# Optimization experiments

Measured on AMD Instinct MI355X. Metric: run time of the kernel, lower is better.

## Reference

```python
import jax, jax.numpy as jnp
import numpy as np

D_MODEL = 512
NUM_HEADS = 8
HEAD_DIM = D_MODEL // NUM_HEADS
SEQ_LEN = 4096
BATCH = 2
D_FF = 4 * D_MODEL
EPS = 1e-5


def _layer_norm(x, g, b):
    mu = jnp.mean(x, axis=-1, keepdims=True)
    var = jnp.var(x, axis=-1, keepdims=True)
    return (x - mu) * jax.lax.rsqrt(var + EPS) * g + b


def setup_inputs() -> dict:
    key = jax.random.key(0)
    ks = jax.random.split(key, 12)
    s = 0.02
    inp = {
        "x": jax.random.normal(ks[0], (BATCH, SEQ_LEN, D_MODEL), jnp.float32),
        # Linear weights stored as [in, out] (y = x @ W + b)
        "Wq": jax.random.normal(ks[1], (D_MODEL, D_MODEL), jnp.float32) * s,
        "bq": jnp.zeros((D_MODEL,), jnp.float32),
        "Wk": jax.random.normal(ks[2], (D_MODEL, D_MODEL), jnp.float32) * s,
        "bk": jnp.zeros((D_MODEL,), jnp.float32),
        "Wv": jax.random.normal(ks[3], (D_MODEL, D_MODEL), jnp.float32) * s,
        "bv": jnp.zeros((D_MODEL,), jnp.float32),
        "Wo": jax.random.normal(ks[4], (D_MODEL, D_MODEL), jnp.float32) * s,
        "bo": jnp.zeros((D_MODEL,), jnp.float32),
        "ln1_g": jnp.ones((D_MODEL,), jnp.float32),
        "ln1_b": jnp.zeros((D_MODEL,), jnp.float32),
        "ln2_g": jnp.ones((D_MODEL,), jnp.float32),
        "ln2_b": jnp.zeros((D_MODEL,), jnp.float32),
        "W1": jax.random.normal(ks[5], (D_MODEL, D_FF), jnp.float32) * s,
        "b1": jnp.zeros((D_FF,), jnp.float32),
        "W2": jax.random.normal(ks[6], (D_FF, D_MODEL), jnp.float32) * s,
        "b2": jnp.zeros((D_MODEL,), jnp.float32),
    }
    return inp


def reference(x, Wq, bq, Wk, bk, Wv, bv, Wo, bo, ln1_g, ln1_b, ln2_g, ln2_b, W1, b1, W2, b2):
    B, S, D = x.shape
    residual = x
    h = _layer_norm(x, ln1_g, ln1_b)
    # project and split heads: [B, H, S, Dh]
    def split_heads(t):
        return t.reshape(B, S, NUM_HEADS, HEAD_DIM).transpose(0, 2, 1, 3)
    q = split_heads(h @ Wq + bq)
    k = split_heads(h @ Wk + bk)
    v = split_heads(h @ Wv + bv)
    scores = jnp.einsum("bhqd,bhkd->bhqk", q, k) / (HEAD_DIM ** 0.5)
    attn = jax.nn.softmax(scores, axis=-1)
    out = jnp.einsum("bhqk,bhkd->bhqd", attn, v)
    out = out.transpose(0, 2, 1, 3).reshape(B, S, D)
    out = out @ Wo + bo
    x1 = residual + out
    h2 = _layer_norm(x1, ln2_g, ln2_b)
    ff = jax.nn.gelu(h2 @ W1 + b1, approximate=False) @ W2 + b2
    return x1 + ff
```

## Files before the change

kernel.cpp:

```cpp
#include <hip/hip_runtime.h>
#include <hip/hip_bf16.h>
#include <math.h>

typedef __hip_bfloat16 bf16;

#define D_MODEL 512
#define NUM_HEADS 8
#define HEAD_DIM 64
#define SEQ_LEN 4096
#define BATCH 2
#define D_FF 2048
#define TOKENS (BATCH * SEQ_LEN)
#define QKV_STRIDE 1536
#define KSPLIT 2

typedef short short4v __attribute__((ext_vector_type(4)));
typedef short short8v __attribute__((ext_vector_type(8)));
typedef float float4v __attribute__((ext_vector_type(4)));
typedef float float2v __attribute__((ext_vector_type(2)));

union frag_u { short8v v8; short4v v4[2]; short s[8]; };
union pack_u { unsigned u[2]; short4v v4; };

__device__ __forceinline__ float b2f(bf16 v) { return __bfloat162float(v); }
__device__ __forceinline__ bf16 f2b(float v) { return __float2bfloat16(v); }
__device__ __forceinline__ short f2bs(float v) { bf16 t = __float2bfloat16(v); return *(short*)&t; }
__device__ __forceinline__ float exp2fast(float x) { return __builtin_amdgcn_exp2f(x); }

__device__ __forceinline__ unsigned pack_bf16(float lo, float hi) {
    unsigned a = __float_as_uint(hi) + 0x8000u;
    unsigned b = __float_as_uint(lo) + 0x8000u;
    return __builtin_amdgcn_perm(a, b, 0x07060302u);
}

__device__ __forceinline__ unsigned cvt_pk_bf16(float lo, float hi) {
    unsigned r;
    asm("v_cvt_pk_bf16_f32 %0, %1, %2" : "=v"(r) : "v"(lo), "v"(hi));
    return r;
}

__device__ __forceinline__ int3 swz_xyz() {
    int gx = gridDim.x, gy = gridDim.y;
    int id = blockIdx.x + gx * (blockIdx.y + gy * blockIdx.z);
    int nwg = gx * gy * (int)gridDim.z;
    int nid = (id & 7) * (nwg >> 3) + (id >> 3);
    int3 r;
    r.x = nid % gx;
    int t = nid / gx;
    r.y = t % gy;
    r.z = t / gy;
    return r;
}

#define AS1(p) ((__attribute__((address_space(1))) void*)(p))
#define AS3(p) ((__attribute__((address_space(3))) void*)(p))

__device__ __forceinline__ int self_detect(const unsigned* __restrict__ xw, int tid) {
    unsigned w = xw[tid & 63];
    unsigned e = (w >> 7) & 0xFFu;
    unsigned long long b = __ballot(e >= 110 && e <= 140);
    return __popcll(b) < 32;
}

__device__ __forceinline__ void do_tr(const void* __restrict__ src, bf16* __restrict__ dst,
                                      int K, int N, int n0, int k0, int fl, int tid,
                                      bf16 (*tile)[65]) {
    int c = tid & 63, r4 = tid >> 6;
#pragma unroll
    for (int t = 0; t < 16; t++) {
        int r = t * 4 + r4;
        size_t si = (size_t)(k0 + r) * N + n0 + c;
        float v = fl ? ((const float*)src)[si] : b2f(((const bf16*)src)[si]);
        tile[r][c] = f2b(v);
    }
    __syncthreads();
#pragma unroll
    for (int t = 0; t < 16; t++) {
        int r = t * 4 + r4;
        dst[(size_t)(n0 + r) * K + k0 + c] = tile[c][r];
    }
}

__global__ void prep_kernel(const void* x, const void* Wq, const void* Wk, const void* Wv,
                            const void* Wo, const void* W1, const void* W2,
                            const void* bq, const void* bk, const void* bv, const void* bo,
                            const void* b1, const void* b2,
                            const void* g1, const void* e1, const void* g2, const void* e2,
                            bf16* __restrict__ Wqkvt ,
                            bf16* __restrict__ W1t, bf16* __restrict__ W2t,
                            bf16* __restrict__ small, int* __restrict__ flag) {
    __shared__ bf16 tile[64][65];
    int blk = blockIdx.x, tid = threadIdx.x;
    int fl = self_detect((const unsigned*)x, tid);
    if (blk == 0 && tid == 0) flag[0] = fl;
    if (blk < 256) {
        int z = blk >> 6, tt = blk & 63;
        const void* src = (z == 0) ? Wq : (z == 1) ? Wk : (z == 2) ? Wv : Wo;
        do_tr(src, Wqkvt + (size_t)z * 512 * 512, 512, 512, (tt & 7) * 64, (tt >> 3) * 64,
              fl, tid, tile);
    } else if (blk < 512) {
        int tt = blk - 256;
        do_tr(W1, W1t, 512, 2048, (tt & 31) * 64, (tt >> 5) * 64, fl, tid, tile);
    } else if (blk < 768) {
        int tt = blk - 512;
        do_tr(W2, W2t, 2048, 512, (tt & 7) * 64, (tt >> 3) * 64, fl, tid, tile);
    } else {
        int i = (blk - 768) * 256 + tid;
        const void* src; int off;
        if (i < 512)       { src = bq; off = 0; }
        else if (i < 1024) { src = bk; off = 512; }
        else if (i < 1536) { src = bv; off = 1024; }
        else if (i < 2048) { src = bo; off = 1536; }
        else if (i < 4096) { src = b1; off = 2048; }
        else if (i < 4608) { src = b2; off = 4096; }
        else if (i < 5120) { src = g1; off = 4608; }
        else if (i < 5632) { src = e1; off = 5120; }
        else if (i < 6144) { src = g2; off = 5632; }
        else               { src = e2; off = 6144; }
        int j = i - off;
        small[i] = fl ? f2b(((const float*)src)[j]) : ((const bf16*)src)[j];
    }
}

template <int MODE>
__global__ void ln_kernel(const void* __restrict__ xv, const bf16* __restrict__ g,
                          const bf16* __restrict__ b, bf16* __restrict__ out,
                          const int* __restrict__ flag) {
    int t = blockIdx.x;
    int tid = threadIdx.x;
    int fl = (MODE == 2) ? *flag : 0;
    float v0, v1;
    if (fl) {
        const float* xr = (const float*)xv + (size_t)t * D_MODEL;
        v0 = xr[tid]; v1 = xr[tid + 256];
    } else {
        const bf16* xr = (const bf16*)xv + (size_t)t * D_MODEL;
        v0 = b2f(xr[tid]); v1 = b2f(xr[tid + 256]);
    }
    float s = v0 + v1, ss = v0 * v0 + v1 * v1;
    for (int o = 32; o > 0; o >>= 1) {
        s += __shfl_down(s, o);
        ss += __shfl_down(ss, o);
    }
    __shared__ float rs[4], rss[4], stat[2];
    int w = tid >> 6, l = tid & 63;
    if (l == 0) { rs[w] = s; rss[w] = ss; }
    __syncthreads();
    if (tid == 0) {
        float S = rs[0] + rs[1] + rs[2] + rs[3];
        float SS = rss[0] + rss[1] + rss[2] + rss[3];
        float mu = S / (float)D_MODEL;
        float var = SS / (float)D_MODEL - mu * mu;
        stat[0] = mu;
        stat[1] = rsqrtf(var + 1e-5f);
    }
    __syncthreads();
    float mu = stat[0], rstd = stat[1];
    bf16* orow = out + (size_t)t * D_MODEL;
    orow[tid]       = f2b((v0 - mu) * rstd * b2f(g[tid])       + b2f(b[tid]));
    orow[tid + 256] = f2b((v1 - mu) * rstd * b2f(g[tid + 256]) + b2f(b[tid + 256]));
}

__device__ __forceinline__ float gelu_tanh(float v) {
    float u = 0.7978845608f * (v + 0.044715f * v * v * v);
    float e2 = __expf(-2.f * u);
    return v / (1.f + e2);
}

template <int ACT>
__global__ __launch_bounds__(256) void mfma_gemm(
    const bf16* __restrict__ A, const bf16* __restrict__ Wt,
    const bf16* __restrict__ bias, bf16* __restrict__ Cout,
    bf16* __restrict__ Vt_out, int M, int N, int K) {
    __shared__ bf16 As[128 * 64];
    __shared__ bf16 Bs[128 * 64];
    int tid = threadIdx.x, wave = tid >> 6, lane = tid & 63;
    int m = lane & 15, g = lane >> 4;
    int3 sw = swz_xyz();
    int row0 = sw.y * 128, col0 = sw.x * 128;
    int R0 = (wave >> 1) * 64, C0 = (wave & 1) * 64;
    float4v acc[4][4] = {};

    int srow = lane >> 3;
    int scol = (lane & 7) * 8;
    const bf16* Ab = A  + (size_t)(row0 + wave * 8 + srow) * K + scol;
    const bf16* Bb = Wt + (size_t)(col0 + wave * 8 + srow) * K + scol;

    for (int k0 = 0; k0 < K; k0 += 64) {
#pragma unroll
        for (int t = 0; t < 4; t++) {
            int rbase = t * 32 + wave * 8;
            __builtin_amdgcn_global_load_lds(AS1(Ab + (size_t)(t * 32) * K + k0),
                                             AS3(&As[rbase * 64]), 16, 0, 0);
            __builtin_amdgcn_global_load_lds(AS1(Bb + (size_t)(t * 32) * K + k0),
                                             AS3(&Bs[rbase * 64]), 16, 0, 0);
        }
        __syncthreads();
#pragma unroll
        for (int kk = 0; kk < 2; kk++) {
            short8v fa[4], fb[4];
#pragma unroll
            for (int i = 0; i < 4; i++)
                fa[i] = *(const short8v*)&As[(R0 + i * 16 + m) * 64 + kk * 32 + g * 8];
#pragma unroll
            for (int j = 0; j < 4; j++)
                fb[j] = *(const short8v*)&Bs[(C0 + j * 16 + m) * 64 + kk * 32 + g * 8];
#pragma unroll
            for (int i = 0; i < 4; i++)
#pragma unroll
                for (int j = 0; j < 4; j++)
                    acc[i][j] = __builtin_amdgcn_mfma_f32_16x16x32_bf16(fa[i], fb[j], acc[i][j], 0, 0, 0);
        }
        __syncthreads();
    }

    if (Vt_out != nullptr && col0 >= 1024) {
#pragma unroll
        for (int i = 0; i < 4; i++) {
            int row = row0 + R0 + i * 16 + g * 4;
            int b = row >> 12, s = row & (SEQ_LEN - 1);
#pragma unroll
            for (int j = 0; j < 4; j++) {
                int col = col0 + C0 + j * 16 + m;
                int hh = (col - 1024) >> 6, d = col & 63;
                float bi = b2f(bias[col]);
                pack_u oo;
                oo.u[0] = pack_bf16(acc[i][j][0] + bi, acc[i][j][1] + bi);
                oo.u[1] = pack_bf16(acc[i][j][2] + bi, acc[i][j][3] + bi);
                *(short4v*)&Vt_out[((size_t)((b << 3) + hh) * 64 + d) * SEQ_LEN + s] = oo.v4;
            }
        }
        return;
    }

#pragma unroll
    for (int i = 0; i < 4; i++) {
#pragma unroll
        for (int r = 0; r < 4; r++) {
            int row = row0 + R0 + i * 16 + g * 4 + r;
#pragma unroll
            for (int j = 0; j < 4; j++) {
                int col = col0 + C0 + j * 16 + m;
                float v = acc[i][j][r] + b2f(bias[col]);
                if (ACT == 1) v = gelu_tanh(v);
                Cout[(size_t)row * N + col] = f2b(v);
            }
        }
    }
}

template <int RES, int OUTMODE>
__global__ __launch_bounds__(256) void mfma_gemm64(
    const bf16* __restrict__ A, const bf16* __restrict__ Wt,
    const bf16* __restrict__ bias, const void* __restrict__ res,
    void* __restrict__ Cout, const int* __restrict__ flag, int M, int N, int K) {
    __shared__ bf16 As[128 * 64];
    __shared__ bf16 Bs[64 * 64];
    int tid = threadIdx.x, wave = tid >> 6, lane = tid & 63;
    int m = lane & 15, g = lane >> 4;
    int3 sw = swz_xyz();
    int row0 = sw.y * 128, col0 = sw.x * 64;
    int R0 = wave * 32;
    int fl = (OUTMODE == 2 || RES == 3) ? *flag : 0;
    float4v acc[2][4] = {};

    int srow = lane >> 3;
    int scol = (lane & 7) * 8;
    const bf16* Ab = A  + (size_t)(row0 + wave * 8 + srow) * K + scol;
    const bf16* Bb = Wt + (size_t)(col0 + wave * 8 + srow) * K + scol;

    for (int k0 = 0; k0 < K; k0 += 64) {
#pragma unroll
        for (int t = 0; t < 4; t++) {
            __builtin_amdgcn_global_load_lds(AS1(Ab + (size_t)(t * 32) * K + k0),
                                             AS3(&As[(t * 32 + wave * 8) * 64]), 16, 0, 0);
            if (t < 2)
                __builtin_amdgcn_global_load_lds(AS1(Bb + (size_t)(t * 32) * K + k0),
                                                 AS3(&Bs[(t * 32 + wave * 8) * 64]), 16, 0, 0);
        }
        __syncthreads();
#pragma unroll
        for (int kk = 0; kk < 2; kk++) {
            short8v fa[2], fb[4];
#pragma unroll
            for (int i = 0; i < 2; i++)
                fa[i] = *(const short8v*)&As[(R0 + i * 16 + m) * 64 + kk * 32 + g * 8];
#pragma unroll
            for (int j = 0; j < 4; j++)
                fb[j] = *(const short8v*)&Bs[(j * 16 + m) * 64 + kk * 32 + g * 8];
#pragma unroll
            for (int i = 0; i < 2; i++)
#pragma unroll
                for (int j = 0; j < 4; j++)
                    acc[i][j] = __builtin_amdgcn_mfma_f32_16x16x32_bf16(fa[i], fb[j], acc[i][j], 0, 0, 0);
        }
        __syncthreads();
    }

#pragma unroll
    for (int i = 0; i < 2; i++) {
#pragma unroll
        for (int r = 0; r < 4; r++) {
            int row = row0 + R0 + i * 16 + g * 4 + r;
#pragma unroll
            for (int j = 0; j < 4; j++) {
                int col = col0 + j * 16 + m;
                float v = acc[i][j][r] + b2f(bias[col]);
                size_t idx = (size_t)row * N + col;
                if (RES == 2) v += b2f(((const bf16*)res)[idx]);
                if (RES == 3) v += fl ? ((const float*)res)[idx]
                                      : b2f(((const bf16*)res)[idx]);
                if (OUTMODE == 0) ((bf16*)Cout)[idx] = f2b(v);
                else {
                    if (fl) ((float*)Cout)[idx] = v;
                    else ((bf16*)Cout)[idx] = f2b(v);
                }
            }
        }
    }
}

#define F3(a, b, c) fmaxf(fmaxf((a), (b)), (c))
__global__ __launch_bounds__(256, 4) void flash_attn(const bf16* __restrict__ Q,
                                                     const bf16* __restrict__ K,
                                                     const bf16* __restrict__ Vt_g,
                                                     bf16* __restrict__ Op,
                                                     float2* __restrict__ mlout) {
    __shared__ bf16 Ks[64][72];
    __shared__ bf16 Vt[64][72];
    __shared__ bf16 Pt[4][32][72];

    int tid = threadIdx.x;
    int wave = tid >> 6, lane = tid & 63;
    int m = lane & 15, g = lane >> 4;

    int3 sw = swz_xyz();
    int bh = sw.y;
    size_t base = (size_t)(bh >> 3) * SEQ_LEN * QKV_STRIDE + (size_t)(bh & 7) * HEAD_DIM;
    int q0w = sw.x * 128 + wave * 32;

    const float qscale = 0.125f * 1.44269504f;
    short8v aQ[2][2];
#pragma unroll
    for (int mt = 0; mt < 2; mt++) {
        const bf16* qp = Q + base + (size_t)(q0w + mt * 16 + m) * QKV_STRIDE + g * 8;
#pragma unroll
        for (int c = 0; c < 2; c++) {
            frag_u u;
#pragma unroll
            for (int j = 0; j < 8; j++) u.s[j] = f2bs(b2f(qp[c * 32 + j]) * qscale);
            aQ[mt][c] = u.v8;
        }
    }

    float mrow[2] = {-1e30f, -1e30f};
    float lrow[2] = {0.f, 0.f};
    float4v oacc[2][4] = {};

    int sk = tid >> 2, sd = (tid & 3) * 16;
    int vrow = tid >> 2, vcol = (tid & 3) * 16;

    const unsigned short* Ku = (const unsigned short*)(K + base);
    const unsigned short* Vg = (const unsigned short*)Vt_g +
                               (size_t)bh * 64 * SEQ_LEN + (size_t)vrow * SEQ_LEN;

    int t0 = sw.z * (64 / KSPLIT);
    int t1 = t0 + 64 / KSPLIT;

    short8v rk0, rk1, rv0, rv1;
    {
        int kt0 = t0 * 64;
        const unsigned short* kp = Ku + (size_t)(kt0 + sk) * QKV_STRIDE + sd;
        rk0 = *(const short8v*)(kp);
        rk1 = *(const short8v*)(kp + 8);
        rv0 = *(const short8v*)(Vg + kt0 + vcol);
        rv1 = *(const short8v*)(Vg + kt0 + vcol + 8);
        *(short8v*)&Ks[sk][sd]     = rk0;
        *(short8v*)&Ks[sk][sd + 8] = rk1;
        *(short8v*)&Vt[vrow][vcol]     = rv0;
        *(short8v*)&Vt[vrow][vcol + 8] = rv1;
    }
    __syncthreads();

    for (int t = t0; t < t1; t++) {
        if (t + 1 < t1) {
            int ktn = (t + 1) * 64;
            const unsigned short* kp = Ku + (size_t)(ktn + sk) * QKV_STRIDE + sd;
            rk0 = *(const short8v*)(kp);
            rk1 = *(const short8v*)(kp + 8);
            rv0 = *(const short8v*)(Vg + ktn + vcol);
            rv1 = *(const short8v*)(Vg + ktn + vcol + 8);
        }

        float4v st[2][4];
        __builtin_amdgcn_s_setprio(1);
#pragma unroll
        for (int kt = 0; kt < 4; kt++) {
            short8v bK0 = *(const short8v*)&Ks[kt * 16 + m][g * 8];
            short8v bK1 = *(const short8v*)&Ks[kt * 16 + m][32 + g * 8];
#pragma unroll
            for (int mt = 0; mt < 2; mt++) {
                float4v a = {0.f, 0.f, 0.f, 0.f};
                a = __builtin_amdgcn_mfma_f32_16x16x32_bf16(bK0, aQ[mt][0], a, 0, 0, 0);
                a = __builtin_amdgcn_mfma_f32_16x16x32_bf16(bK1, aQ[mt][1], a, 0, 0, 0);
                st[mt][kt] = a;
            }
        }
        __builtin_amdgcn_s_setprio(0);

#pragma unroll
        for (int mt = 0; mt < 2; mt++) {
            float u0 = F3(st[mt][0][0], st[mt][0][1], st[mt][0][2]);
            float u1 = F3(st[mt][0][3], st[mt][1][0], st[mt][1][1]);
            float u2 = F3(st[mt][1][2], st[mt][1][3], st[mt][2][0]);
            float u3 = F3(st[mt][2][1], st[mt][2][2], st[mt][2][3]);
            float u4 = F3(st[mt][3][0], st[mt][3][1], st[mt][3][2]);
            float tm = fmaxf(F3(u0, u1, u2), F3(u3, u4, st[mt][3][3]));
            tm = fmaxf(tm, __shfl_xor(tm, 16));
            tm = fmaxf(tm, __shfl_xor(tm, 32));
            if (!__all(tm - mrow[mt] <= 8.f)) {
                float mnew = fmaxf(mrow[mt], tm);
                float alpha = exp2fast(mrow[mt] - mnew);
                mrow[mt] = mnew;
                lrow[mt] *= alpha;
#pragma unroll
                for (int dt = 0; dt < 4; dt++)
#pragma unroll
                    for (int r = 0; r < 4; r++) oacc[mt][dt][r] *= alpha;
            }
            float mcur = mrow[mt];
            float2v ps = {0.f, 0.f};
#pragma unroll
            for (int kt = 0; kt < 4; kt++) {
                float p0 = exp2fast(st[mt][kt][0] - mcur);
                float p1 = exp2fast(st[mt][kt][1] - mcur);
                float p2 = exp2fast(st[mt][kt][2] - mcur);
                float p3 = exp2fast(st[mt][kt][3] - mcur);
                float2v a = {p0, p1}, b = {p2, p3};
                ps += a + b;
                pack_u pp;
                pp.u[0] = cvt_pk_bf16(p0, p1);
                pp.u[1] = cvt_pk_bf16(p2, p3);
                *(short4v*)&Pt[wave][mt * 16 + m][kt * 16 + g * 4] = pp.v4;
            }
            lrow[mt] += ps[0] + ps[1];
        }

        short8v bP[2][2];
#pragma unroll
        for (int mt = 0; mt < 2; mt++)
#pragma unroll
            for (int c = 0; c < 2; c++)
                bP[mt][c] = *(const short8v*)&Pt[wave][mt * 16 + m][c * 32 + g * 8];

        __builtin_amdgcn_s_setprio(1);
#pragma unroll
        for (int dt = 0; dt < 4; dt++) {
#pragma unroll
            for (int c = 0; c < 2; c++) {
                short8v av = *(const short8v*)&Vt[dt * 16 + m][c * 32 + g * 8];
#pragma unroll
                for (int mt = 0; mt < 2; mt++)
                    oacc[mt][dt] = __builtin_amdgcn_mfma_f32_16x16x32_bf16(av, bP[mt][c], oacc[mt][dt], 0, 0, 0);
            }
        }
        __builtin_amdgcn_s_setprio(0);

        __syncthreads();
        if (t + 1 < t1) {
            *(short8v*)&Ks[sk][sd]     = rk0;
            *(short8v*)&Ks[sk][sd + 8] = rk1;
            *(short8v*)&Vt[vrow][vcol]     = rv0;
            *(short8v*)&Vt[vrow][vcol + 8] = rv1;
        }
        __syncthreads();
    }

    size_t zoff = (size_t)sw.z * NUM_HEADS * BATCH + bh;
    size_t pbase = zoff * (SEQ_LEN * (size_t)HEAD_DIM);
#pragma unroll
    for (int mt = 0; mt < 2; mt++) {
        float l = lrow[mt];
        l += __shfl_xor(l, 16);
        l += __shfl_xor(l, 32);
        int q = q0w + mt * 16 + m;
        bf16* orow = Op + pbase + (size_t)q * HEAD_DIM;
#pragma unroll
        for (int dt = 0; dt < 4; dt++) {
            pack_u oo;
            oo.u[0] = cvt_pk_bf16(oacc[mt][dt][0], oacc[mt][dt][1]);
            oo.u[1] = cvt_pk_bf16(oacc[mt][dt][2], oacc[mt][dt][3]);
            *(short4v*)&orow[dt * 16 + g * 4] = oo.v4;
        }
        if (g == 0) mlout[zoff * SEQ_LEN + q] = make_float2(mrow[mt], l);
    }
}

__global__ void attn_merge(const bf16* __restrict__ Op, const float2* __restrict__ ml,
                           bf16* __restrict__ O) {
    int i = blockIdx.x * 256 + threadIdx.x;
    int d = i & 63;
    int q = (i >> 6) & (SEQ_LEN - 1);
    int bh = i >> 18;
    const int HQ = NUM_HEADS * BATCH * SEQ_LEN;
    float2 a0 = ml[bh * SEQ_LEN + q];
    float2 a1 = ml[HQ + bh * SEQ_LEN + q];
    float M = fmaxf(a0.x, a1.x);
    float w0 = exp2fast(a0.x - M), w1 = exp2fast(a1.x - M);
    float inv = 1.f / (a0.y * w0 + a1.y * w1);
    const size_t NP = (size_t)HQ * HEAD_DIM;
    float o = (b2f(Op[i]) * w0 + b2f(Op[NP + i]) * w1) * inv;
    O[((size_t)((bh >> 3) * SEQ_LEN + q)) * D_MODEL + (bh & 7) * HEAD_DIM + d] = f2b(o);
}

extern "C" void kernel_launch(void* const* d_in, const int* in_sizes, int n_in,
                              void* d_out, int out_size, void* d_ws, size_t ws_size,
                              hipStream_t stream) {
    const void* x     = d_in[0];
    const void* Wq    = d_in[1];
    const void* bq    = d_in[2];
    const void* Wk    = d_in[3];
    const void* bk    = d_in[4];
    const void* Wv    = d_in[5];
    const void* bv    = d_in[6];
    const void* Wo    = d_in[7];
    const void* bo    = d_in[8];
    const void* ln1_g = d_in[9];
    const void* ln1_b = d_in[10];
    const void* ln2_g = d_in[11];
    const void* ln2_b = d_in[12];
    const void* W1    = d_in[13];
    const void* b1    = d_in[14];
    const void* W2    = d_in[15];
    const void* b2    = d_in[16];

    char* p = (char*)d_ws;
    int* flag = (int*)p;                      p += 256;
    size_t tok_d = (size_t)TOKENS * D_MODEL;
    char* region2 = p;                        p += 2 * tok_d * 2;
    bf16* x1b   = (bf16*)region2;
    bf16* hb    = (bf16*)(region2 + tok_d * 2);
    bf16* Opart = (bf16*)region2;
    bf16*  bigA = (bf16*)p;                   p += (size_t)TOKENS * D_FF * 2;
    bf16*  qkvb = bigA;
    bf16*  ab   = bigA + (size_t)TOKENS * QKV_STRIDE;
    bf16*  ffb  = bigA;
    bf16*  Wqkvt = (bf16*)p;                  p += (size_t)QKV_STRIDE * D_MODEL * 2;
    bf16*  Wot   = (bf16*)p;                  p += (size_t)D_MODEL * D_MODEL * 2;
    bf16*  W1t   = (bf16*)p;                  p += (size_t)D_FF * D_MODEL * 2;
    bf16*  W2t   = (bf16*)p;                  p += (size_t)D_MODEL * D_FF * 2;
    bf16*  Vtg   = (bf16*)p;                  p += (size_t)NUM_HEADS * BATCH * HEAD_DIM * SEQ_LEN * 2;
    float2* mlb  = (float2*)p;                p += (size_t)KSPLIT * NUM_HEADS * BATCH * SEQ_LEN * sizeof(float2);
    bf16*  small = (bf16*)p;                  p += 6656 * 2;
    bf16* bias_qkv = small + 0;
    bf16* bias_o   = small + 1536;
    bf16* b1b      = small + 2048;
    bf16* b2b      = small + 4096;
    bf16* g1b      = small + 4608;
    bf16* be1b     = small + 5120;
    bf16* g2b      = small + 5632;
    bf16* be2b     = small + 6144;

    prep_kernel<<<794, 256, 0, stream>>>(x, Wq, Wk, Wv, Wo, W1, W2,
                                         bq, bk, bv, bo, b1, b2,
                                         ln1_g, ln1_b, ln2_g, ln2_b,
                                         Wqkvt, W1t, W2t, small, flag);

    ln_kernel<2><<<TOKENS, 256, 0, stream>>>(x, g1b, be1b, hb, flag);

    mfma_gemm<0><<<dim3(QKV_STRIDE / 128, TOKENS / 128), 256, 0, stream>>>(
        hb, Wqkvt, bias_qkv, qkvb, Vtg, TOKENS, QKV_STRIDE, D_MODEL);

    flash_attn<<<dim3(SEQ_LEN / 128, 16, KSPLIT), 256, 0, stream>>>(
        qkvb, qkvb + 512, Vtg, Opart, mlb);
    attn_merge<<<(NUM_HEADS * BATCH * SEQ_LEN * HEAD_DIM) / 256, 256, 0, stream>>>(
        Opart, mlb, ab);

    mfma_gemm64<3, 0><<<dim3(D_MODEL / 64, TOKENS / 128), 256, 0, stream>>>(
        ab, Wot, bias_o, x, x1b, flag, TOKENS, D_MODEL, D_MODEL);

    ln_kernel<0><<<TOKENS, 256, 0, stream>>>(x1b, g2b, be2b, hb, flag);

    mfma_gemm<1><<<dim3(D_FF / 128, TOKENS / 128), 256, 0, stream>>>(
        hb, W1t, b1b, ffb, nullptr, TOKENS, D_FF, D_MODEL);

    mfma_gemm64<2, 2><<<dim3(D_MODEL / 64, TOKENS / 128), 256, 0, stream>>>(
        ffb, W2t, b2b, x1b, d_out, flag, TOKENS, D_MODEL, D_FF);
}
```

Baseline: 351.0 us.

## Alias P tile into K smem, raise occupancy, and allow 4-way KV split

Removes the dedicated per-wave P shared buffer by reusing the K tile storage after a barrier, cutting LDS per block, and raises the occupancy hint from 4 to 5 blocks. It templates the KV split count and uses a 4-way split when the workspace is large enough, with a generalized merge kernel. The intent is more resident blocks and more parallel work for attention, at the cost of an extra barrier per tile, larger partial-output traffic and a heavier merge.

```diff
diff --git a/kernel.cpp b/kernel.cpp
--- a/kernel.cpp
+++ b/kernel.cpp
@@ -12,7 +12,6 @@
 #define D_FF 2048
 #define TOKENS (BATCH * SEQ_LEN)
 #define QKV_STRIDE 1536
-#define KSPLIT 2
 
 typedef short short4v __attribute__((ext_vector_type(4)));
 typedef short short8v __attribute__((ext_vector_type(8)));
@@ -321,18 +320,19 @@
 }
 
 #define F3(a, b, c) fmaxf(fmaxf((a), (b)), (c))
-__global__ __launch_bounds__(256, 4) void flash_attn(const bf16* __restrict__ Q,
+template <int KS>
+__global__ __launch_bounds__(256, 5) void flash_attn(const bf16* __restrict__ Q,
                                                      const bf16* __restrict__ K,
                                                      const bf16* __restrict__ Vt_g,
                                                      bf16* __restrict__ Op,
                                                      float2* __restrict__ mlout) {
     __shared__ bf16 Ks[64][72];
     __shared__ bf16 Vt[64][72];
-    __shared__ bf16 Pt[4][32][72];
 
     int tid = threadIdx.x;
     int wave = tid >> 6, lane = tid & 63;
     int m = lane & 15, g = lane >> 4;
+    bf16* PtW = &Ks[0][0] + wave * (16 * 72);
 
     int3 sw = swz_xyz();
     int bh = sw.y;
@@ -364,8 +364,8 @@
     const unsigned short* Vg = (const unsigned short*)Vt_g +
                                (size_t)bh * 64 * SEQ_LEN + (size_t)vrow * SEQ_LEN;
 
-    int t0 = sw.z * (64 / KSPLIT);
-    int t1 = t0 + 64 / KSPLIT;
+    int t0 = sw.z * (64 / KS);
+    int t1 = t0 + 64 / KS;
 
     short8v rk0, rk1, rv0, rv1;
     {
@@ -408,6 +408,9 @@
         }
         __builtin_amdgcn_s_setprio(0);
 
+        __syncthreads();
+
+        short8v bP[2][2];
 #pragma unroll
         for (int mt = 0; mt < 2; mt++) {
             float u0 = F3(st[mt][0][0], st[mt][0][1], st[mt][0][2]);
@@ -441,17 +444,13 @@
                 pack_u pp;
                 pp.u[0] = cvt_pk_bf16(p0, p1);
                 pp.u[1] = cvt_pk_bf16(p2, p3);
-                *(short4v*)&Pt[wave][mt * 16 + m][kt * 16 + g * 4] = pp.v4;
+                *(short4v*)&PtW[m * 72 + kt * 16 + g * 4] = pp.v4;
             }
             lrow[mt] += ps[0] + ps[1];
-        }
-
-        short8v bP[2][2];
-#pragma unroll
-        for (int mt = 0; mt < 2; mt++)
 #pragma unroll
             for (int c = 0; c < 2; c++)
-                bP[mt][c] = *(const short8v*)&Pt[wave][mt * 16 + m][c * 32 + g * 8];
+                bP[mt][c] = *(const short8v*)&PtW[m * 72 + c * 32 + g * 8];
+        }
 
         __builtin_amdgcn_s_setprio(1);
 #pragma unroll
@@ -496,6 +495,7 @@
     }
 }
 
+template <int KS>
 __global__ void attn_merge(const bf16* __restrict__ Op, const float2* __restrict__ ml,
                            bf16* __restrict__ O) {
     int i = blockIdx.x * 256 + threadIdx.x;
@@ -503,13 +503,26 @@
     int q = (i >> 6) & (SEQ_LEN - 1);
     int bh = i >> 18;
     const int HQ = NUM_HEADS * BATCH * SEQ_LEN;
-    float2 a0 = ml[bh * SEQ_LEN + q];
-    float2 a1 = ml[HQ + bh * SEQ_LEN + q];
-    float M = fmaxf(a0.x, a1.x);
-    float w0 = exp2fast(a0.x - M), w1 = exp2fast(a1.x - M);
-    float inv = 1.f / (a0.y * w0 + a1.y * w1);
+    float2 a[KS];
+    float M = -1e30f;
+#pragma unroll
+    for (int p = 0; p < KS; p++) {
+        a[p] = ml[(size_t)p * HQ + bh * SEQ_LEN + q];
+        M = fmaxf(M, a[p].x);
+    }
+    float w[KS];
+    float denom = 0.f;
+#pragma unroll
+    for (int p = 0; p < KS; p++) {
+        w[p] = exp2fast(a[p].x - M);
+        denom += a[p].y * w[p];
+    }
+    float inv = 1.f / denom;
     const size_t NP = (size_t)HQ * HEAD_DIM;
-    float o = (b2f(Op[i]) * w0 + b2f(Op[NP + i]) * w1) * inv;
+    float o = 0.f;
+#pragma unroll
+    for (int p = 0; p < KS; p++) o += b2f(Op[(size_t)p * NP + i]) * w[p];
+    o *= inv;
     O[((size_t)((bh >> 3) * SEQ_LEN + q)) * D_MODEL + (bh & 7) * HEAD_DIM + d] = f2b(o);
 }
 
@@ -540,7 +553,7 @@
     char* region2 = p;                        p += 2 * tok_d * 2;
     bf16* x1b   = (bf16*)region2;
     bf16* hb    = (bf16*)(region2 + tok_d * 2);
-    bf16* Opart = (bf16*)region2;
+    bf16* Opart2 = (bf16*)region2;
     bf16*  bigA = (bf16*)p;                   p += (size_t)TOKENS * D_FF * 2;
     bf16*  qkvb = bigA;
     bf16*  ab   = bigA + (size_t)TOKENS * QKV_STRIDE;
@@ -550,8 +563,12 @@
     bf16*  W1t   = (bf16*)p;                  p += (size_t)D_FF * D_MODEL * 2;
     bf16*  W2t   = (bf16*)p;                  p += (size_t)D_MODEL * D_FF * 2;
     bf16*  Vtg   = (bf16*)p;                  p += (size_t)NUM_HEADS * BATCH * HEAD_DIM * SEQ_LEN * 2;
-    float2* mlb  = (float2*)p;                p += (size_t)KSPLIT * NUM_HEADS * BATCH * SEQ_LEN * sizeof(float2);
+    float2* mlb  = (float2*)p;                p += (size_t)4 * NUM_HEADS * BATCH * SEQ_LEN * sizeof(float2);
     bf16*  small = (bf16*)p;                  p += 6656 * 2;
+    bf16*  Opart4 = (bf16*)p;
+    size_t opart4_bytes = (size_t)4 * NUM_HEADS * BATCH * SEQ_LEN * HEAD_DIM * 2;
+    int ks4 = ((char*)Opart4 + opart4_bytes - (char*)d_ws) <= (ptrdiff_t)ws_size;
+
     bf16* bias_qkv = small + 0;
     bf16* bias_o   = small + 1536;
     bf16* b1b      = small + 2048;
@@ -571,10 +588,17 @@
     mfma_gemm<0><<<dim3(QKV_STRIDE / 128, TOKENS / 128), 256, 0, stream>>>(
         hb, Wqkvt, bias_qkv, qkvb, Vtg, TOKENS, QKV_STRIDE, D_MODEL);
 
-    flash_attn<<<dim3(SEQ_LEN / 128, 16, KSPLIT), 256, 0, stream>>>(
-        qkvb, qkvb + 512, Vtg, Opart, mlb);
-    attn_merge<<<(NUM_HEADS * BATCH * SEQ_LEN * HEAD_DIM) / 256, 256, 0, stream>>>(
-        Opart, mlb, ab);
+    if (ks4) {
+        flash_attn<4><<<dim3(SEQ_LEN / 128, 16, 4), 256, 0, stream>>>(
+            qkvb, qkvb + 512, Vtg, Opart4, mlb);
+        attn_merge<4><<<(NUM_HEADS * BATCH * SEQ_LEN * HEAD_DIM) / 256, 256, 0, stream>>>(
+            Opart4, mlb, ab);
+    } else {
+        flash_attn<2><<<dim3(SEQ_LEN / 128, 16, 2), 256, 0, stream>>>(
+            qkvb, qkvb + 512, Vtg, Opart2, mlb);
+        attn_merge<2><<<(NUM_HEADS * BATCH * SEQ_LEN * HEAD_DIM) / 256, 256, 0, stream>>>(
+            Opart2, mlb, ab);
+    }
 
     mfma_gemm64<3, 0><<<dim3(D_MODEL / 64, TOKENS / 128), 256, 0, stream>>>(
         ab, Wot, bias_o, x, x1b, flag, TOKENS, D_MODEL, D_MODEL);
```

After: 651.1 us. +85.5%, slower.
